# Performance work log

Measured on AMD Instinct MI355X. Metric: run time of the kernel, lower is better.

## Reference

```python
import jax, jax.numpy as jnp
import numpy as np
from jax import lax

GAMMA = 0.99
LAM = 0.95
CLIP_PARAM = 0.2
VALUE_LOSS_COEF = 0.5
ENTROPY_COEF = 0.01
EPS = 1e-09

B, T = 4096, 2048


def setup_inputs() -> dict:
    key = jax.random.key(0)
    ks = jax.random.split(key, 6)
    rewards = jax.random.normal(ks[0], (B, T), dtype=jnp.float32)
    values = jax.random.normal(ks[1], (B, T + 1), dtype=jnp.float32)
    ref_probs = jax.random.uniform(ks[2], (B, T), dtype=jnp.float32)
    old_probs = jax.random.uniform(ks[3], (B, T), dtype=jnp.float32)
    curr_probs = jax.random.uniform(ks[4], (B, T), dtype=jnp.float32)
    # episode-continuation masks: mostly 1, occasional 0 (episode boundary)
    masks = (jax.random.uniform(ks[5], (B, T)) > 0.02).astype(jnp.float32)
    return {"rewards": rewards, "values": values, "ref_probs": ref_probs,
            "old_probs": old_probs, "curr_probs": curr_probs, "masks": masks}


def compute_gae(rewards, values, masks, gamma, lam):
    # single fused reverse scan over time; per-step state is (B,)
    def step(carry, xs):
        r, v, v_next, m = xs
        delta = r + gamma * v_next * m - v
        adv = delta + gamma * lam * m * carry
        return adv, adv

    xs = (rewards.T, values[:, :-1].T, values[:, 1:].T, masks.T)  # each (T, B)
    _, advs = lax.scan(step, jnp.zeros(rewards.shape[0], rewards.dtype), xs, reverse=True)
    advantages = advs.T  # (B, T)
    returns = advantages + values[:, :-1]
    return advantages, returns


def reference(rewards, values, ref_probs, old_probs, curr_probs, masks):
    advantages, returns = compute_gae(rewards, values, masks, GAMMA, LAM)
    # torch .std() is unbiased (ddof=1)
    advantages = (advantages - advantages.mean()) / (advantages.std(ddof=1) + EPS)
    ratios = curr_probs / (old_probs + EPS)
    surr1 = ratios * advantages
    surr2 = jnp.clip(ratios, 1.0 - CLIP_PARAM, 1.0 + CLIP_PARAM) * advantages
    ppo_loss = -jnp.minimum(surr1, surr2).mean()
    value_loss = jnp.mean((returns - values[:, :-1]) ** 2)
    entropy_loss = -jnp.mean(curr_probs * jnp.log(curr_probs + EPS))
    total_loss = ppo_loss + VALUE_LOSS_COEF * value_loss + ENTROPY_COEF * entropy_loss
    return (total_loss, ppo_loss, VALUE_LOSS_COEF * value_loss, ENTROPY_COEF * entropy_loss)
```

## Files before the change

kernel.cpp:

```cpp
#include <hip/hip_runtime.h>
#include <math.h>


#define GAMMA     0.99f
#define LAM       0.95f
#define CLIP_LO   0.8f
#define CLIP_HI   1.2f
#define EPSF      1e-9f

constexpr int BB = 4096;
constexpr int TT = 2048;
constexpr long long NN = (long long)BB * TT;
constexpr int PPO_BLOCKS = 2048;

struct Stats { float mean; float inv; double sum2; };
static constexpr size_t GAE_PART_OFF = 64;
static constexpr size_t PPO_PART_OFF = 64 + 4096 * sizeof(float2);
static constexpr size_t ADV_OFF      = PPO_PART_OFF + 2048 * sizeof(float2);

__global__ __launch_bounds__(256, 8) void gae_kernel(
    const float* __restrict__ rewards,
    const float* __restrict__ values,
    const float* __restrict__ masks,
    float* __restrict__ adv_out,
    float2* __restrict__ partials)
{
    const int row  = blockIdx.x;
    const int tid  = threadIdx.x;
    const int lane = tid & 63;
    const int wave = tid >> 6;
    const int t0   = tid * 8;

    __shared__ float  lv[2052];
    __shared__ float2 wT[4];
    __shared__ float  wr1[4], wr2[4];

    const float* rrow = rewards + (size_t)row * TT;
    const float* mrow = masks   + (size_t)row * TT;
    const float* vrow = values  + (size_t)row * (TT + 1);

    float4 r0 = *(const float4*)(rrow + t0);
    float4 r1 = *(const float4*)(rrow + t0 + 4);
    float4 m0 = *(const float4*)(mrow + t0);
    float4 m1 = *(const float4*)(mrow + t0 + 4);

#pragma unroll
    for (int k = 0; k < 8; ++k) lv[tid + 256 * k] = vrow[tid + 256 * k];
    if (tid == 0) lv[2048] = vrow[2048];
    __syncthreads();

    float r[8] = {r0.x, r0.y, r0.z, r0.w, r1.x, r1.y, r1.z, r1.w};
    float m[8] = {m0.x, m0.y, m0.z, m0.w, m1.x, m1.y, m1.z, m1.w};
    float v[9];
#pragma unroll
    for (int j = 0; j < 9; ++j) v[j] = lv[t0 + j];

    float delta[8], c[8];
#pragma unroll
    for (int j = 0; j < 8; ++j) {
        delta[j] = r[j] + GAMMA * v[j + 1] * m[j] - v[j];
        c[j]     = (GAMMA * LAM) * m[j];
    }

    float la[8], S[8];
    la[7] = delta[7];
    S[7]  = c[7];
#pragma unroll
    for (int j = 6; j >= 0; --j) {
        la[j] = delta[j] + c[j] * la[j + 1];
        S[j]  = c[j] * S[j + 1];
    }

    float A = S[0], Bv = la[0];
#pragma unroll
    for (int d = 1; d < 64; d <<= 1) {
        float A2 = __shfl_down(A,  d, 64);
        float B2 = __shfl_down(Bv, d, 64);
        if (lane + d < 64) {
            Bv = Bv + A * B2;
            A  = A * A2;
        }
    }
    if (lane == 0) wT[wave] = make_float2(A, Bv);
    __syncthreads();
    float C = 0.0f;
    for (int ww = 3; ww > wave; --ww)
        C = wT[ww].y + wT[ww].x * C;

    float A1 = __shfl_down(A,  1, 64);
    float B1 = __shfl_down(Bv, 1, 64);
    float carry = (lane < 63) ? (B1 + A1 * C) : C;

    float a[8], s1 = 0.f, s2 = 0.f;
#pragma unroll
    for (int j = 0; j < 8; ++j) {
        a[j] = la[j] + S[j] * carry;
        s1 += a[j];
        s2 += a[j] * a[j];
    }
    float4 o0 = {a[0], a[1], a[2], a[3]};
    float4 o1 = {a[4], a[5], a[6], a[7]};
    *(float4*)(adv_out + (size_t)row * TT + t0)     = o0;
    *(float4*)(adv_out + (size_t)row * TT + t0 + 4) = o1;

#pragma unroll
    for (int off = 32; off > 0; off >>= 1) {
        s1 += __shfl_down(s1, off, 64);
        s2 += __shfl_down(s2, off, 64);
    }
    if (lane == 0) { wr1[wave] = s1; wr2[wave] = s2; }
    __syncthreads();
    if (tid == 0) {
        float2 p = {wr1[0] + wr1[1] + wr1[2] + wr1[3],
                    wr2[0] + wr2[1] + wr2[2] + wr2[3]};
        partials[row] = p;
    }
}

__global__ __launch_bounds__(256) void finalize_stats(
    const float2* __restrict__ gp, Stats* __restrict__ stats)
{
    const int tid = threadIdx.x;
    __shared__ double l1[256], l2[256];
    double s1 = 0.0, s2 = 0.0;
    for (int i = tid; i < BB; i += 256) {
        float2 p = gp[i];
        s1 += (double)p.x;
        s2 += (double)p.y;
    }
    l1[tid] = s1; l2[tid] = s2;
    __syncthreads();
    for (int st = 128; st > 0; st >>= 1) {
        if (tid < st) { l1[tid] += l1[tid + st]; l2[tid] += l2[tid + st]; }
        __syncthreads();
    }
    if (tid == 0) {
        double S1 = l1[0], S2 = l2[0];
        double mean = S1 / (double)NN;
        double var  = (S2 - S1 * S1 / (double)NN) / (double)(NN - 1);
        stats->mean = (float)mean;
        stats->inv  = (float)(1.0 / (sqrt(var) + 1e-9));
        stats->sum2 = S2;
    }
}

__global__ __launch_bounds__(256, 4) void ppo_kernel(
    const float* __restrict__ adv,
    const float* __restrict__ oldp,
    const float* __restrict__ currp,
    const Stats* __restrict__ stats,
    float2* __restrict__ partials)
{
    const float mean = stats->mean;
    const float inv  = stats->inv;
    const int tid = threadIdx.x;

    const long long base   = (long long)blockIdx.x * 256 + tid;
    const long long stride = (long long)PPO_BLOCKS * 256;

    const float4* a4 = (const float4*)adv;
    const float4* o4 = (const float4*)oldp;
    const float4* c4 = (const float4*)currp;

    float4 Af[4], Of[4], Cf[4];
#pragma unroll
    for (int k = 0; k < 4; ++k) {
        long long i = base + (long long)k * stride;
        Af[k] = a4[i]; Of[k] = o4[i]; Cf[k] = c4[i];
    }

    float sm = 0.f, se = 0.f;
#pragma unroll
    for (int k = 0; k < 4; ++k) {
        float av[4] = {Af[k].x, Af[k].y, Af[k].z, Af[k].w};
        float ov[4] = {Of[k].x, Of[k].y, Of[k].z, Of[k].w};
        float cv[4] = {Cf[k].x, Cf[k].y, Cf[k].z, Cf[k].w};
#pragma unroll
        for (int j = 0; j < 4; ++j) {
            float an    = (av[j] - mean) * inv;
            float ratio = cv[j] * __builtin_amdgcn_rcpf(ov[j] + EPSF);
            float rc    = fminf(fmaxf(ratio, CLIP_LO), CLIP_HI);
            sm += fminf(ratio * an, rc * an);
            se += cv[j] * __logf(cv[j] + EPSF);
        }
    }

#pragma unroll
    for (int off = 32; off > 0; off >>= 1) {
        sm += __shfl_down(sm, off, 64);
        se += __shfl_down(se, off, 64);
    }
    __shared__ float w1[4], w2[4];
    const int wave = tid >> 6, lane = tid & 63;
    if (lane == 0) { w1[wave] = sm; w2[wave] = se; }
    __syncthreads();
    if (tid == 0) {
        float2 p = {w1[0] + w1[1] + w1[2] + w1[3],
                    w2[0] + w2[1] + w2[2] + w2[3]};
        partials[blockIdx.x] = p;
    }
}

__global__ __launch_bounds__(256) void finalize_out(
    const float2* __restrict__ pp,
    const Stats* __restrict__ stats,
    float* __restrict__ out)
{
    const int tid = threadIdx.x;
    __shared__ double l1[256], l2[256];
    double s1 = 0.0, s2 = 0.0;
    for (int i = tid; i < PPO_BLOCKS; i += 256) {
        float2 p = pp[i];
        s1 += (double)p.x;
        s2 += (double)p.y;
    }
    l1[tid] = s1; l2[tid] = s2;
    __syncthreads();
    for (int st = 128; st > 0; st >>= 1) {
        if (tid < st) { l1[tid] += l1[tid + st]; l2[tid] += l2[tid + st]; }
        __syncthreads();
    }
    if (tid == 0) {
        double invN = 1.0 / (double)NN;
        double vl   = 0.5  * (stats->sum2 * invN);
        double ppo  = -(l1[0] * invN);
        double ent  = -0.01 * (l2[0] * invN);
        out[0] = (float)(ppo + vl + ent);
        out[1] = (float)ppo;
        out[2] = (float)vl;
        out[3] = (float)ent;
    }
}

extern "C" void kernel_launch(void* const* d_in, const int* in_sizes, int n_in,
                              void* d_out, int out_size, void* d_ws, size_t ws_size,
                              hipStream_t stream) {
    const float* rewards = (const float*)d_in[0];
    const float* values  = (const float*)d_in[1];
    const float* oldp    = (const float*)d_in[3];
    const float* currp   = (const float*)d_in[4];
    const float* masks   = (const float*)d_in[5];

    Stats*  stats = (Stats*)d_ws;
    float2* gaep  = (float2*)((char*)d_ws + GAE_PART_OFF);
    float2* ppop  = (float2*)((char*)d_ws + PPO_PART_OFF);
    float*  advws = (float*)((char*)d_ws + ADV_OFF);
    float*  out   = (float*)d_out;

    gae_kernel<<<BB, 256, 0, stream>>>(rewards, values, masks, advws, gaep);
    finalize_stats<<<1, 256, 0, stream>>>(gaep, stats);
    ppo_kernel<<<PPO_BLOCKS, 256, 0, stream>>>(advws, oldp, currp, stats, ppop);
    finalize_out<<<1, 256, 0, stream>>>(ppop, stats, out);
}
```

Measured before the change: 210.7 us.

## Store intermediate advantages as bf16 and process two GAE rows per block

The GAE kernel now handles two rows per block and reads values straight from global memory instead of staging them in LDS. It writes the intermediate advantages as packed bf16 with round-to-nearest-even, halving the write and re-read traffic between the GAE and PPO kernels. The PPO kernel reads contiguous per-block chunks of the bf16 buffer and unpacks them to float. The risk is reduced precision in the PPO loss term, and per-thread unaligned scalar loads of values may be less efficient than the old staged copy.

```diff
diff --git a/kernel.cpp b/kernel.cpp
--- a/kernel.cpp
+++ b/kernel.cpp
@@ -11,97 +11,127 @@
 constexpr int BB = 4096;
 constexpr int TT = 2048;
 constexpr long long NN = (long long)BB * TT;
+constexpr int GAE_BLOCKS = BB / 2;
 constexpr int PPO_BLOCKS = 2048;
 
 struct Stats { float mean; float inv; double sum2; };
 static constexpr size_t GAE_PART_OFF = 64;
-static constexpr size_t PPO_PART_OFF = 64 + 4096 * sizeof(float2);
-static constexpr size_t ADV_OFF      = PPO_PART_OFF + 2048 * sizeof(float2);
-
-__global__ __launch_bounds__(256, 8) void gae_kernel(
+static constexpr size_t PPO_PART_OFF = GAE_PART_OFF + GAE_BLOCKS * sizeof(float2);
+static constexpr size_t ADV_OFF      = PPO_PART_OFF + PPO_BLOCKS * sizeof(float2);
+
+__device__ __forceinline__ unsigned bf16_rne(float x) {
+    unsigned u = __float_as_uint(x);
+    u += 0x7FFFu + ((u >> 16) & 1u);
+    return u >> 16;
+}
+
+__global__ __launch_bounds__(256, 4) void gae_kernel(
     const float* __restrict__ rewards,
     const float* __restrict__ values,
     const float* __restrict__ masks,
-    float* __restrict__ adv_out,
+    uint4* __restrict__ advb,
     float2* __restrict__ partials)
 {
-    const int row  = blockIdx.x;
     const int tid  = threadIdx.x;
     const int lane = tid & 63;
     const int wave = tid >> 6;
     const int t0   = tid * 8;
-
-    __shared__ float  lv[2052];
-    __shared__ float2 wT[4];
+    const int row0 = blockIdx.x * 2;
+    const int row1 = row0 + 1;
+
+    __shared__ float2 wTa[4], wTb[4];
     __shared__ float  wr1[4], wr2[4];
 
-    const float* rrow = rewards + (size_t)row * TT;
-    const float* mrow = masks   + (size_t)row * TT;
-    const float* vrow = values  + (size_t)row * (TT + 1);
-
-    float4 r0 = *(const float4*)(rrow + t0);
-    float4 r1 = *(const float4*)(rrow + t0 + 4);
-    float4 m0 = *(const float4*)(mrow + t0);
-    float4 m1 = *(const float4*)(mrow + t0 + 4);
-
-#pragma unroll
-    for (int k = 0; k < 8; ++k) lv[tid + 256 * k] = vrow[tid + 256 * k];
-    if (tid == 0) lv[2048] = vrow[2048];
-    __syncthreads();
-
-    float r[8] = {r0.x, r0.y, r0.z, r0.w, r1.x, r1.y, r1.z, r1.w};
-    float m[8] = {m0.x, m0.y, m0.z, m0.w, m1.x, m1.y, m1.z, m1.w};
-    float v[9];
-#pragma unroll
-    for (int j = 0; j < 9; ++j) v[j] = lv[t0 + j];
-
-    float delta[8], c[8];
+    const float* ra = rewards + (size_t)row0 * TT;
+    const float* ma = masks   + (size_t)row0 * TT;
+    const float* va_ = values + (size_t)row0 * (TT + 1);
+    const float* rb = rewards + (size_t)row1 * TT;
+    const float* mb = masks   + (size_t)row1 * TT;
+    const float* vb_ = values + (size_t)row1 * (TT + 1);
+
+    float4 ra0 = *(const float4*)(ra + t0);
+    float4 ra1 = *(const float4*)(ra + t0 + 4);
+    float4 ma0 = *(const float4*)(ma + t0);
+    float4 ma1 = *(const float4*)(ma + t0 + 4);
+    float4 rb0 = *(const float4*)(rb + t0);
+    float4 rb1 = *(const float4*)(rb + t0 + 4);
+    float4 mb0 = *(const float4*)(mb + t0);
+    float4 mb1 = *(const float4*)(mb + t0 + 4);
+    float va[9], vb[9];
+#pragma unroll
+    for (int j = 0; j < 9; ++j) va[j] = va_[t0 + j];
+#pragma unroll
+    for (int j = 0; j < 9; ++j) vb[j] = vb_[t0 + j];
+
+    float rA[8] = {ra0.x, ra0.y, ra0.z, ra0.w, ra1.x, ra1.y, ra1.z, ra1.w};
+    float mA[8] = {ma0.x, ma0.y, ma0.z, ma0.w, ma1.x, ma1.y, ma1.z, ma1.w};
+    float rB[8] = {rb0.x, rb0.y, rb0.z, rb0.w, rb1.x, rb1.y, rb1.z, rb1.w};
+    float mB[8] = {mb0.x, mb0.y, mb0.z, mb0.w, mb1.x, mb1.y, mb1.z, mb1.w};
+
+    float laA[8], SA[8], laB[8], SB[8];
+    {
+        float d[8], c[8];
+#pragma unroll
+        for (int j = 0; j < 8; ++j) {
+            d[j] = rA[j] + GAMMA * va[j + 1] * mA[j] - va[j];
+            c[j] = (GAMMA * LAM) * mA[j];
+        }
+        laA[7] = d[7]; SA[7] = c[7];
+#pragma unroll
+        for (int j = 6; j >= 0; --j) { laA[j] = d[j] + c[j] * laA[j + 1]; SA[j] = c[j] * SA[j + 1]; }
+    }
+    {
+        float d[8], c[8];
+#pragma unroll
+        for (int j = 0; j < 8; ++j) {
+            d[j] = rB[j] + GAMMA * vb[j + 1] * mB[j] - vb[j];
+            c[j] = (GAMMA * LAM) * mB[j];
+        }
+        laB[7] = d[7]; SB[7] = c[7];
+#pragma unroll
+        for (int j = 6; j >= 0; --j) { laB[j] = d[j] + c[j] * laB[j + 1]; SB[j] = c[j] * SB[j + 1]; }
+    }
+
+    float Aa = SA[0], Ba = laA[0];
+    float Ab = SB[0], Bb = laB[0];
+#pragma unroll
+    for (int d = 1; d < 64; d <<= 1) {
+        float A2a = __shfl_down(Aa, d, 64), B2a = __shfl_down(Ba, d, 64);
+        float A2b = __shfl_down(Ab, d, 64), B2b = __shfl_down(Bb, d, 64);
+        if (lane + d < 64) {
+            Ba = Ba + Aa * B2a;  Aa = Aa * A2a;
+            Bb = Bb + Ab * B2b;  Ab = Ab * A2b;
+        }
+    }
+    if (lane == 0) { wTa[wave] = make_float2(Aa, Ba); wTb[wave] = make_float2(Ab, Bb); }
+    __syncthreads();
+    float Ca = 0.0f, Cb = 0.0f;
+    for (int ww = 3; ww > wave; --ww) {
+        Ca = wTa[ww].y + wTa[ww].x * Ca;
+        Cb = wTb[ww].y + wTb[ww].x * Cb;
+    }
+    float A1a = __shfl_down(Aa, 1, 64), B1a = __shfl_down(Ba, 1, 64);
+    float A1b = __shfl_down(Ab, 1, 64), B1b = __shfl_down(Bb, 1, 64);
+    float carA = (lane < 63) ? (B1a + A1a * Ca) : Ca;
+    float carB = (lane < 63) ? (B1b + A1b * Cb) : Cb;
+
+    float s1 = 0.f, s2 = 0.f;
+    unsigned ha[8], hb[8];
 #pragma unroll
     for (int j = 0; j < 8; ++j) {
-        delta[j] = r[j] + GAMMA * v[j + 1] * m[j] - v[j];
-        c[j]     = (GAMMA * LAM) * m[j];
-    }
-
-    float la[8], S[8];
-    la[7] = delta[7];
-    S[7]  = c[7];
-#pragma unroll
-    for (int j = 6; j >= 0; --j) {
-        la[j] = delta[j] + c[j] * la[j + 1];
-        S[j]  = c[j] * S[j + 1];
-    }
-
-    float A = S[0], Bv = la[0];
-#pragma unroll
-    for (int d = 1; d < 64; d <<= 1) {
-        float A2 = __shfl_down(A,  d, 64);
-        float B2 = __shfl_down(Bv, d, 64);
-        if (lane + d < 64) {
-            Bv = Bv + A * B2;
-            A  = A * A2;
-        }
-    }
-    if (lane == 0) wT[wave] = make_float2(A, Bv);
-    __syncthreads();
-    float C = 0.0f;
-    for (int ww = 3; ww > wave; --ww)
-        C = wT[ww].y + wT[ww].x * C;
-
-    float A1 = __shfl_down(A,  1, 64);
-    float B1 = __shfl_down(Bv, 1, 64);
-    float carry = (lane < 63) ? (B1 + A1 * C) : C;
-
-    float a[8], s1 = 0.f, s2 = 0.f;
-#pragma unroll
-    for (int j = 0; j < 8; ++j) {
-        a[j] = la[j] + S[j] * carry;
-        s1 += a[j];
-        s2 += a[j] * a[j];
-    }
-    float4 o0 = {a[0], a[1], a[2], a[3]};
-    float4 o1 = {a[4], a[5], a[6], a[7]};
-    *(float4*)(adv_out + (size_t)row * TT + t0)     = o0;
-    *(float4*)(adv_out + (size_t)row * TT + t0 + 4) = o1;
+        float a = laA[j] + SA[j] * carA;
+        s1 += a; s2 += a * a;
+        ha[j] = bf16_rne(a);
+        float b = laB[j] + SB[j] * carB;
+        s1 += b; s2 += b * b;
+        hb[j] = bf16_rne(b);
+    }
+    uint4 pa = {ha[0] | (ha[1] << 16), ha[2] | (ha[3] << 16),
+                ha[4] | (ha[5] << 16), ha[6] | (ha[7] << 16)};
+    uint4 pb = {hb[0] | (hb[1] << 16), hb[2] | (hb[3] << 16),
+                hb[4] | (hb[5] << 16), hb[6] | (hb[7] << 16)};
+    advb[row0 * 256 + tid] = pa;
+    advb[row1 * 256 + tid] = pb;
 
 #pragma unroll
     for (int off = 32; off > 0; off >>= 1) {
@@ -113,7 +143,7 @@
     if (tid == 0) {
         float2 p = {wr1[0] + wr1[1] + wr1[2] + wr1[3],
                     wr2[0] + wr2[1] + wr2[2] + wr2[3]};
-        partials[row] = p;
+        partials[blockIdx.x] = p;
     }
 }
 
@@ -123,7 +153,7 @@
     const int tid = threadIdx.x;
     __shared__ double l1[256], l2[256];
     double s1 = 0.0, s2 = 0.0;
-    for (int i = tid; i < BB; i += 256) {
+    for (int i = tid; i < GAE_BLOCKS; i += 256) {
         float2 p = gp[i];
         s1 += (double)p.x;
         s2 += (double)p.y;
@@ -144,8 +174,8 @@
     }
 }
 
-__global__ __launch_bounds__(256, 4) void ppo_kernel(
-    const float* __restrict__ adv,
+__global__ __launch_bounds__(256, 8) void ppo_kernel(
+    const float* __restrict__ adv_bf16,
     const float* __restrict__ oldp,
     const float* __restrict__ currp,
     const Stats* __restrict__ stats,
@@ -154,25 +184,26 @@
     const float mean = stats->mean;
     const float inv  = stats->inv;
     const int tid = threadIdx.x;
-
-    const long long base   = (long long)blockIdx.x * 256 + tid;
-    const long long stride = (long long)PPO_BLOCKS * 256;
-
-    const float4* a4 = (const float4*)adv;
+    const int b   = blockIdx.x;
+
+    const uint2*  a2 = (const uint2*)adv_bf16;
     const float4* o4 = (const float4*)oldp;
     const float4* c4 = (const float4*)currp;
 
-    float4 Af[4], Of[4], Cf[4];
+    uint2  Aq[4]; float4 Of[4], Cf[4];
 #pragma unroll
     for (int k = 0; k < 4; ++k) {
-        long long i = base + (long long)k * stride;
-        Af[k] = a4[i]; Of[k] = o4[i]; Cf[k] = c4[i];
+        int i = b * 1024 + k * 256 + tid;
+        Aq[k] = a2[i]; Of[k] = o4[i]; Cf[k] = c4[i];
     }
 
     float sm = 0.f, se = 0.f;
 #pragma unroll
     for (int k = 0; k < 4; ++k) {
-        float av[4] = {Af[k].x, Af[k].y, Af[k].z, Af[k].w};
+        float av[4] = {__uint_as_float(Aq[k].x << 16),
+                       __uint_as_float(Aq[k].x & 0xFFFF0000u),
+                       __uint_as_float(Aq[k].y << 16),
+                       __uint_as_float(Aq[k].y & 0xFFFF0000u)};
         float ov[4] = {Of[k].x, Of[k].y, Of[k].z, Of[k].w};
         float cv[4] = {Cf[k].x, Cf[k].y, Cf[k].z, Cf[k].w};
 #pragma unroll
@@ -197,7 +228,7 @@
     if (tid == 0) {
         float2 p = {w1[0] + w1[1] + w1[2] + w1[3],
                     w2[0] + w2[1] + w2[2] + w2[3]};
-        partials[blockIdx.x] = p;
+        partials[b] = p;
     }
 }
 
@@ -244,11 +275,11 @@
     Stats*  stats = (Stats*)d_ws;
     float2* gaep  = (float2*)((char*)d_ws + GAE_PART_OFF);
     float2* ppop  = (float2*)((char*)d_ws + PPO_PART_OFF);
-    float*  advws = (float*)((char*)d_ws + ADV_OFF);
+    uint4*  advb  = (uint4*)((char*)d_ws + ADV_OFF);
     float*  out   = (float*)d_out;
 
-    gae_kernel<<<BB, 256, 0, stream>>>(rewards, values, masks, advws, gaep);
+    gae_kernel<<<GAE_BLOCKS, 256, 0, stream>>>(rewards, values, masks, advb, gaep);
     finalize_stats<<<1, 256, 0, stream>>>(gaep, stats);
-    ppo_kernel<<<PPO_BLOCKS, 256, 0, stream>>>(advws, oldp, currp, stats, ppop);
+    ppo_kernel<<<PPO_BLOCKS, 256, 0, stream>>>((const float*)advb, oldp, currp, stats, ppop);
     finalize_out<<<1, 256, 0, stream>>>(ppop, stats, out);
 }
```

New measurement: 203.5 us. 3.4% less time.

## Store advantages as bf16, one wave per GAE row, fold stats finalize into PPO

Applied to the files above, without the earlier changes.

The GAE kernel now gives each wave its own row. It walks the row in eight chunks with register prefetch and carries the scan value between chunks, so it no longer needs LDS staging or block-wide barriers. The advantage intermediate is written in bf16 instead of fp32, which halves the write-then-read traffic between the two passes. The separate stats-finalize launch is removed: every PPO block redundantly reduces the 4096 GAE partials itself. The costs are the precision loss on normalized advantages from bf16 storage, the extra per-block reduction work, and a more serial scan per wave.

```diff
diff --git a/kernel.cpp b/kernel.cpp
--- a/kernel.cpp
+++ b/kernel.cpp
@@ -11,168 +11,163 @@
 constexpr int BB = 4096;
 constexpr int TT = 2048;
 constexpr long long NN = (long long)BB * TT;
+constexpr int GAE_BLOCKS = BB / 4;
 constexpr int PPO_BLOCKS = 2048;
 
-struct Stats { float mean; float inv; double sum2; };
 static constexpr size_t GAE_PART_OFF = 64;
-static constexpr size_t PPO_PART_OFF = 64 + 4096 * sizeof(float2);
-static constexpr size_t ADV_OFF      = PPO_PART_OFF + 2048 * sizeof(float2);
-
-__global__ __launch_bounds__(256, 8) void gae_kernel(
+static constexpr size_t PPO_PART_OFF = GAE_PART_OFF + BB * sizeof(float2);
+static constexpr size_t ADV_OFF      = PPO_PART_OFF + PPO_BLOCKS * sizeof(float2);
+
+__device__ __forceinline__ unsigned bf16_rne(float x) {
+    unsigned u = __float_as_uint(x);
+    u += 0x7FFFu + ((u >> 16) & 1u);
+    return u >> 16;
+}
+
+__global__ __launch_bounds__(256, 4) void gae_kernel(
     const float* __restrict__ rewards,
     const float* __restrict__ values,
     const float* __restrict__ masks,
-    float* __restrict__ adv_out,
+    uint2* __restrict__ advb,
     float2* __restrict__ partials)
 {
-    const int row  = blockIdx.x;
     const int tid  = threadIdx.x;
     const int lane = tid & 63;
     const int wave = tid >> 6;
-    const int t0   = tid * 8;
-
-    __shared__ float  lv[2052];
-    __shared__ float2 wT[4];
-    __shared__ float  wr1[4], wr2[4];
+    const int row  = blockIdx.x * 4 + wave;
 
     const float* rrow = rewards + (size_t)row * TT;
     const float* mrow = masks   + (size_t)row * TT;
     const float* vrow = values  + (size_t)row * (TT + 1);
 
-    float4 r0 = *(const float4*)(rrow + t0);
-    float4 r1 = *(const float4*)(rrow + t0 + 4);
-    float4 m0 = *(const float4*)(mrow + t0);
-    float4 m1 = *(const float4*)(mrow + t0 + 4);
-
-#pragma unroll
-    for (int k = 0; k < 8; ++k) lv[tid + 256 * k] = vrow[tid + 256 * k];
-    if (tid == 0) lv[2048] = vrow[2048];
-    __syncthreads();
-
-    float r[8] = {r0.x, r0.y, r0.z, r0.w, r1.x, r1.y, r1.z, r1.w};
-    float m[8] = {m0.x, m0.y, m0.z, m0.w, m1.x, m1.y, m1.z, m1.w};
-    float v[9];
-#pragma unroll
-    for (int j = 0; j < 9; ++j) v[j] = lv[t0 + j];
-
-    float delta[8], c[8];
-#pragma unroll
-    for (int j = 0; j < 8; ++j) {
-        delta[j] = r[j] + GAMMA * v[j + 1] * m[j] - v[j];
-        c[j]     = (GAMMA * LAM) * m[j];
-    }
-
-    float la[8], S[8];
-    la[7] = delta[7];
-    S[7]  = c[7];
-#pragma unroll
-    for (int j = 6; j >= 0; --j) {
-        la[j] = delta[j] + c[j] * la[j + 1];
-        S[j]  = c[j] * S[j + 1];
-    }
-
-    float A = S[0], Bv = la[0];
-#pragma unroll
-    for (int d = 1; d < 64; d <<= 1) {
-        float A2 = __shfl_down(A,  d, 64);
-        float B2 = __shfl_down(Bv, d, 64);
-        if (lane + d < 64) {
-            Bv = Bv + A * B2;
-            A  = A * A2;
-        }
-    }
-    if (lane == 0) wT[wave] = make_float2(A, Bv);
-    __syncthreads();
-    float C = 0.0f;
-    for (int ww = 3; ww > wave; --ww)
-        C = wT[ww].y + wT[ww].x * C;
-
-    float A1 = __shfl_down(A,  1, 64);
-    float B1 = __shfl_down(Bv, 1, 64);
-    float carry = (lane < 63) ? (B1 + A1 * C) : C;
-
-    float a[8], s1 = 0.f, s2 = 0.f;
-#pragma unroll
-    for (int j = 0; j < 8; ++j) {
-        a[j] = la[j] + S[j] * carry;
-        s1 += a[j];
-        s2 += a[j] * a[j];
-    }
-    float4 o0 = {a[0], a[1], a[2], a[3]};
-    float4 o1 = {a[4], a[5], a[6], a[7]};
-    *(float4*)(adv_out + (size_t)row * TT + t0)     = o0;
-    *(float4*)(adv_out + (size_t)row * TT + t0 + 4) = o1;
+    int e = 256 * 7 + 4 * lane;
+    float4 rc = *(const float4*)(rrow + e);
+    float4 mc = *(const float4*)(mrow + e);
+    float vc0 = vrow[e], vc1 = vrow[e + 1], vc2 = vrow[e + 2], vc3 = vrow[e + 3];
+    float head = vrow[2048];
+
+    float V  = 0.0f;
+    float s1 = 0.f, s2 = 0.f;
+
+    for (int k = 7; k >= 0; --k) {
+        float4 rn, mn;
+        float vn0 = 0.f, vn1 = 0.f, vn2 = 0.f, vn3 = 0.f;
+        if (k > 0) {
+            const int en = 256 * (k - 1) + 4 * lane;
+            rn  = *(const float4*)(rrow + en);
+            mn  = *(const float4*)(mrow + en);
+            vn0 = vrow[en]; vn1 = vrow[en + 1]; vn2 = vrow[en + 2]; vn3 = vrow[en + 3];
+        }
+
+        float v4 = __shfl_down(vc0, 1, 64);
+        if (lane == 63) v4 = head;
+        float nexthead = __shfl(vc0, 0, 64);
+
+        float vv[5] = {vc0, vc1, vc2, vc3, v4};
+        float rr[4] = {rc.x, rc.y, rc.z, rc.w};
+        float mm[4] = {mc.x, mc.y, mc.z, mc.w};
+        float la[4], S[4];
+        {
+            float d[4], c[4];
+#pragma unroll
+            for (int j = 0; j < 4; ++j) {
+                d[j] = rr[j] + GAMMA * vv[j + 1] * mm[j] - vv[j];
+                c[j] = (GAMMA * LAM) * mm[j];
+            }
+            la[3] = d[3]; S[3] = c[3];
+#pragma unroll
+            for (int j = 2; j >= 0; --j) {
+                la[j] = d[j] + c[j] * la[j + 1];
+                S[j]  = c[j] * S[j + 1];
+            }
+        }
+
+        float A = S[0], Bv = la[0];
+#pragma unroll
+        for (int d = 1; d < 64; d <<= 1) {
+            float A2 = __shfl_down(A,  d, 64);
+            float B2 = __shfl_down(Bv, d, 64);
+            if (lane + d < 64) { Bv = Bv + A * B2; A = A * A2; }
+        }
+        float A1 = __shfl_down(A,  1, 64);
+        float B1 = __shfl_down(Bv, 1, 64);
+        float carry = (lane < 63) ? (B1 + A1 * V) : V;
+
+        float a0 = la[0] + S[0] * carry;
+        float a1 = la[1] + S[1] * carry;
+        float a2 = la[2] + S[2] * carry;
+        float a3 = la[3] + S[3] * carry;
+        s1 += a0 + a1 + a2 + a3;
+        s2 += a0 * a0 + a1 * a1 + a2 * a2 + a3 * a3;
+
+        uint2 pk = {bf16_rne(a0) | (bf16_rne(a1) << 16),
+                    bf16_rne(a2) | (bf16_rne(a3) << 16)};
+        advb[(size_t)row * 512 + 64 * k + lane] = pk;
+
+        float vtmp = Bv + A * V;
+        V    = __shfl(vtmp, 0, 64);
+        head = nexthead;
+
+        rc = rn; mc = mn;
+        vc0 = vn0; vc1 = vn1; vc2 = vn2; vc3 = vn3;
+    }
 
 #pragma unroll
     for (int off = 32; off > 0; off >>= 1) {
         s1 += __shfl_down(s1, off, 64);
         s2 += __shfl_down(s2, off, 64);
     }
-    if (lane == 0) { wr1[wave] = s1; wr2[wave] = s2; }
-    __syncthreads();
-    if (tid == 0) {
-        float2 p = {wr1[0] + wr1[1] + wr1[2] + wr1[3],
-                    wr2[0] + wr2[1] + wr2[2] + wr2[3]};
-        partials[row] = p;
-    }
-}
-
-__global__ __launch_bounds__(256) void finalize_stats(
-    const float2* __restrict__ gp, Stats* __restrict__ stats)
+    if (lane == 0) partials[row] = make_float2(s1, s2);
+}
+
+__global__ __launch_bounds__(256, 4) void ppo_kernel(
+    const float* __restrict__ adv_bf16,
+    const float* __restrict__ oldp,
+    const float* __restrict__ currp,
+    const float2* __restrict__ gaep,
+    float2* __restrict__ partials)
 {
     const int tid = threadIdx.x;
+    const int b   = blockIdx.x;
+
     __shared__ double l1[256], l2[256];
-    double s1 = 0.0, s2 = 0.0;
-    for (int i = tid; i < BB; i += 256) {
-        float2 p = gp[i];
-        s1 += (double)p.x;
-        s2 += (double)p.y;
-    }
-    l1[tid] = s1; l2[tid] = s2;
-    __syncthreads();
-    for (int st = 128; st > 0; st >>= 1) {
-        if (tid < st) { l1[tid] += l1[tid + st]; l2[tid] += l2[tid + st]; }
+    {
+        double d1 = 0.0, d2 = 0.0;
+        for (int i = tid; i < BB; i += 256) {
+            float2 p = gaep[i];
+            d1 += (double)p.x;
+            d2 += (double)p.y;
+        }
+        l1[tid] = d1; l2[tid] = d2;
         __syncthreads();
-    }
-    if (tid == 0) {
-        double S1 = l1[0], S2 = l2[0];
-        double mean = S1 / (double)NN;
-        double var  = (S2 - S1 * S1 / (double)NN) / (double)(NN - 1);
-        stats->mean = (float)mean;
-        stats->inv  = (float)(1.0 / (sqrt(var) + 1e-9));
-        stats->sum2 = S2;
-    }
-}
-
-__global__ __launch_bounds__(256, 4) void ppo_kernel(
-    const float* __restrict__ adv,
-    const float* __restrict__ oldp,
-    const float* __restrict__ currp,
-    const Stats* __restrict__ stats,
-    float2* __restrict__ partials)
-{
-    const float mean = stats->mean;
-    const float inv  = stats->inv;
-    const int tid = threadIdx.x;
-
-    const long long base   = (long long)blockIdx.x * 256 + tid;
-    const long long stride = (long long)PPO_BLOCKS * 256;
-
-    const float4* a4 = (const float4*)adv;
+        for (int st = 128; st > 0; st >>= 1) {
+            if (tid < st) { l1[tid] += l1[tid + st]; l2[tid] += l2[tid + st]; }
+            __syncthreads();
+        }
+    }
+    const double S1 = l1[0], S2 = l2[0];
+    const double var = (S2 - S1 * S1 / (double)NN) / (double)(NN - 1);
+    const float mean = (float)(S1 / (double)NN);
+    const float inv  = (float)(1.0 / (sqrt(var) + 1e-9));
+
+    const uint2*  a2 = (const uint2*)adv_bf16;
     const float4* o4 = (const float4*)oldp;
     const float4* c4 = (const float4*)currp;
 
-    float4 Af[4], Of[4], Cf[4];
+    uint2  Aq[4]; float4 Of[4], Cf[4];
 #pragma unroll
     for (int k = 0; k < 4; ++k) {
-        long long i = base + (long long)k * stride;
-        Af[k] = a4[i]; Of[k] = o4[i]; Cf[k] = c4[i];
+        int i = b * 1024 + k * 256 + tid;
+        Aq[k] = a2[i]; Of[k] = o4[i]; Cf[k] = c4[i];
     }
 
     float sm = 0.f, se = 0.f;
 #pragma unroll
     for (int k = 0; k < 4; ++k) {
-        float av[4] = {Af[k].x, Af[k].y, Af[k].z, Af[k].w};
+        float av[4] = {__uint_as_float(Aq[k].x << 16),
+                       __uint_as_float(Aq[k].x & 0xFFFF0000u),
+                       __uint_as_float(Aq[k].y << 16),
+                       __uint_as_float(Aq[k].y & 0xFFFF0000u)};
         float ov[4] = {Of[k].x, Of[k].y, Of[k].z, Of[k].w};
         float cv[4] = {Cf[k].x, Cf[k].y, Cf[k].z, Cf[k].w};
 #pragma unroll
@@ -197,32 +192,37 @@
     if (tid == 0) {
         float2 p = {w1[0] + w1[1] + w1[2] + w1[3],
                     w2[0] + w2[1] + w2[2] + w2[3]};
-        partials[blockIdx.x] = p;
+        partials[b] = p;
     }
 }
 
 __global__ __launch_bounds__(256) void finalize_out(
     const float2* __restrict__ pp,
-    const Stats* __restrict__ stats,
+    const float2* __restrict__ gaep,
     float* __restrict__ out)
 {
     const int tid = threadIdx.x;
-    __shared__ double l1[256], l2[256];
-    double s1 = 0.0, s2 = 0.0;
+    __shared__ double l1[256], l2[256], l3[256];
+    double s1 = 0.0, s2 = 0.0, s3 = 0.0;
     for (int i = tid; i < PPO_BLOCKS; i += 256) {
         float2 p = pp[i];
         s1 += (double)p.x;
         s2 += (double)p.y;
     }
-    l1[tid] = s1; l2[tid] = s2;
+    for (int i = tid; i < BB; i += 256) s3 += (double)gaep[i].y;
+    l1[tid] = s1; l2[tid] = s2; l3[tid] = s3;
     __syncthreads();
     for (int st = 128; st > 0; st >>= 1) {
-        if (tid < st) { l1[tid] += l1[tid + st]; l2[tid] += l2[tid + st]; }
+        if (tid < st) {
+            l1[tid] += l1[tid + st];
+            l2[tid] += l2[tid + st];
+            l3[tid] += l3[tid + st];
+        }
         __syncthreads();
     }
     if (tid == 0) {
         double invN = 1.0 / (double)NN;
-        double vl   = 0.5  * (stats->sum2 * invN);
+        double vl   = 0.5  * (l3[0] * invN);
         double ppo  = -(l1[0] * invN);
         double ent  = -0.01 * (l2[0] * invN);
         out[0] = (float)(ppo + vl + ent);
@@ -241,14 +241,12 @@
     const float* currp   = (const float*)d_in[4];
     const float* masks   = (const float*)d_in[5];
 
-    Stats*  stats = (Stats*)d_ws;
-    float2* gaep  = (float2*)((char*)d_ws + GAE_PART_OFF);
-    float2* ppop  = (float2*)((char*)d_ws + PPO_PART_OFF);
-    float*  advws = (float*)((char*)d_ws + ADV_OFF);
-    float*  out   = (float*)d_out;
-
-    gae_kernel<<<BB, 256, 0, stream>>>(rewards, values, masks, advws, gaep);
-    finalize_stats<<<1, 256, 0, stream>>>(gaep, stats);
-    ppo_kernel<<<PPO_BLOCKS, 256, 0, stream>>>(advws, oldp, currp, stats, ppop);
-    finalize_out<<<1, 256, 0, stream>>>(ppop, stats, out);
-}
+    float2* gaep = (float2*)((char*)d_ws + GAE_PART_OFF);
+    float2* ppop = (float2*)((char*)d_ws + PPO_PART_OFF);
+    uint2*  advb = (uint2*)((char*)d_ws + ADV_OFF);
+    float*  out  = (float*)d_out;
+
+    gae_kernel<<<GAE_BLOCKS, 256, 0, stream>>>(rewards, values, masks, advb, gaep);
+    ppo_kernel<<<PPO_BLOCKS, 256, 0, stream>>>((const float*)advb, oldp, currp, gaep, ppop);
+    finalize_out<<<1, 256, 0, stream>>>(ppop, gaep, out);
+}
```

Measured after the change: 211.9 us. No clear change (+0.6%).
